# Kernel optimization log

Hardware: AMD Instinct MI355X
Metric: run time of the kernel (lower is better)

The kernel has to match this reference:

```python
import jax, jax.numpy as jnp
import numpy as np
from jax import lax

SEQ, B, I, H, O = 512, 64, 512, 1024, 512


def _linear_params(key, out_f, in_f):
    kw, kb = jax.random.split(key)
    bound = 1.0 / np.sqrt(in_f)
    W = jax.random.uniform(kw, (out_f, in_f), jnp.float32, -bound, bound)
    b = jax.random.uniform(kb, (out_f,), jnp.float32, -bound, bound)
    return W, b


def setup_inputs() -> dict:
    key = jax.random.key(0)
    ks = jax.random.split(key, 8)
    x = jax.random.normal(ks[0], (SEQ, B, I), jnp.float32)
    Wxz, bxz = _linear_params(ks[1], H, I)
    Whz, bhz = _linear_params(ks[2], H, H)
    Wxr, bxr = _linear_params(ks[3], H, I)
    Whr, bhr = _linear_params(ks[4], H, H)
    Wxh, bxh = _linear_params(ks[5], H, I)
    Whh, bhh = _linear_params(ks[6], H, H)
    Why, bhy = _linear_params(ks[7], O, H)
    return {"x": x, "Wxz": Wxz, "bxz": bxz, "Whz": Whz, "bhz": bhz,
            "Wxr": Wxr, "bxr": bxr, "Whr": Whr, "bhr": bhr,
            "Wxh": Wxh, "bxh": bxh, "Whh": Whh, "bhh": bhh,
            "Why": Why, "bhy": bhy}


def reference(x, Wxz, bxz, Whz, bhz, Wxr, bxr, Whr, bhr, Wxh, bxh, Whh, bhh, Why, bhy):
    # Precompute all input-side projections in batched GEMMs: [S,B,H]
    xz = jnp.einsum('sbi,hi->sbh', x, Wxz) + bxz
    xr = jnp.einsum('sbi,hi->sbh', x, Wxr) + bxr
    xh = jnp.einsum('sbi,hi->sbh', x, Wxh) + bxh

    def step(h, inp):
        xz_t, xr_t, xh_t = inp
        z = jax.nn.sigmoid(xz_t + h @ Whz.T + bhz)
        r = jax.nn.sigmoid(xr_t + h @ Whr.T + bhr)
        h_cand = jnp.tanh(xh_t + r * (h @ Whh.T + bhh))
        h_new = (1.0 - z) * h + z * h_cand
        return h_new, h_new

    h0 = jnp.zeros((x.shape[1], Whz.shape[0]), x.dtype)
    _, hs = lax.scan(step, h0, (xz, xr, xh))  # hs: [S,B,H]
    out = jnp.einsum('sbh,oh->sbo', hs, Why) + bhy  # [S,B,O]
    return out
```

## Files before the change

### kernel.cpp

```cpp
#include <hip/hip_runtime.h>
#include <hip/hip_bf16.h>

#define SEQL 512
#define BATCH 64
#define INF 512
#define HID 1024
#define OUTF 512
#define SB (SEQL*BATCH)
#define BH (BATCH*HID)

typedef __attribute__((ext_vector_type(8))) __bf16 bf16x8;
typedef __attribute__((ext_vector_type(4))) float f32x4;

__device__ inline bf16x8 ld_bf8(const void* p) { return *reinterpret_cast<const bf16x8*>(p); }
__device__ inline unsigned short f2bf(float f) { __bf16 b = (__bf16)f; return __builtin_bit_cast(unsigned short, b); }

__device__ inline void st_u64c(void* p, unsigned long long v) {
    __hip_atomic_store((unsigned long long*)p, v, __ATOMIC_RELAXED, __HIP_MEMORY_SCOPE_AGENT);
}

__global__ void cvt_f32_bf16(const float* __restrict__ src, unsigned short* __restrict__ dst, int n) {
    int i = (blockIdx.x * blockDim.x + threadIdx.x) * 4;
    if (i < n) {
        float4 v = *reinterpret_cast<const float4*>(src + i);
        ushort4 o = make_ushort4(f2bf(v.x), f2bf(v.y), f2bf(v.z), f2bf(v.w));
        *reinterpret_cast<ushort4*>(dst + i) = o;
    }
}

__global__ void make_bias2(const float* bxz, const float* bhz, const float* bxr,
                           const float* bhr, float* bias2) {
    int i = blockIdx.x * blockDim.x + threadIdx.x;
    if (i < HID) bias2[i] = bxz[i] + bhz[i];
    else if (i < 2*HID) bias2[i] = bxr[i-HID] + bhr[i-HID];
}

__global__ void fail_sentinel(float* o) { o[0] = 1e9f; }

__global__ __launch_bounds__(256, 2) void gemm_nt_f32(
        const unsigned short* __restrict__ A,
        const unsigned short* __restrict__ Bw, int ldb,
        const float* __restrict__ bias,
        float* __restrict__ Cf, int N, int K) {
    __shared__ __align__(16) char lds[32768];
    const int tid = threadIdx.x;
    const int ntn = N >> 7;
    const int bm = blockIdx.x / ntn, bn = blockIdx.x % ntn;
    const int rowbase = bm << 7, colbase = bn << 7;
    const int wave = tid >> 6, lane = tid & 63, lo = lane & 15, hi = lane >> 4;
    const int vm = wave >> 1, vn = wave & 1;

    auto stage = [&](int abase, int k0) {
        #pragma unroll
        for (int i = 0; i < 2; i++) {
            int linear = i * 256 + tid;
            int r = linear >> 2, s = linear & 3;
            int c = (s - (r >> 1)) & 3;
            int R = rowbase + r;
            const unsigned short* ga = A + ((size_t)(R >> 6) * 65536 + (size_t)((R >> 4) & 3) * 16384
                                     + (size_t)((((k0 + c * 8) >> 3) * 16) + (R & 15)) * 8);
            const unsigned short* gb = Bw + (size_t)(colbase + r) * ldb + k0 + c * 8;
            __builtin_amdgcn_global_load_lds(
                (const __attribute__((address_space(1))) unsigned int*)ga,
                (__attribute__((address_space(3))) unsigned int*)(lds + abase + linear * 16), 16, 0, 0);
            __builtin_amdgcn_global_load_lds(
                (const __attribute__((address_space(1))) unsigned int*)gb,
                (__attribute__((address_space(3))) unsigned int*)(lds + 16384 + abase + linear * 16), 16, 0, 0);
        }
    };

    f32x4 acc[4][4] = {};
    const int nk = K >> 5;
    stage(0, 0);
    for (int kt = 0; kt < nk; kt++) {
        __syncthreads();
        if (kt + 1 < nk) stage(((kt + 1) & 1) * 8192, (kt + 1) << 5);
        const char* cA = lds + (kt & 1) * 8192;
        const char* cB = lds + 16384 + (kt & 1) * 8192;
        bf16x8 af[4], bfr[4];
        #pragma unroll
        for (int m = 0; m < 4; m++) {
            int r = vm * 64 + m * 16 + lo;
            af[m] = ld_bf8(cA + r * 64 + 16 * ((hi + (r >> 1)) & 3));
        }
        #pragma unroll
        for (int n = 0; n < 4; n++) {
            int r = vn * 64 + n * 16 + lo;
            bfr[n] = ld_bf8(cB + r * 64 + 16 * ((hi + (r >> 1)) & 3));
        }
        #pragma unroll
        for (int m = 0; m < 4; m++)
            #pragma unroll
            for (int n = 0; n < 4; n++)
                acc[m][n] = __builtin_amdgcn_mfma_f32_16x16x32_bf16(af[m], bfr[n], acc[m][n], 0, 0, 0);
        __syncthreads();
    }

    #pragma unroll
    for (int n = 0; n < 4; n++) {
        int col = colbase + vn * 64 + n * 16 + lo;
        float bv = bias[col];
        #pragma unroll
        for (int m = 0; m < 4; m++)
            #pragma unroll
            for (int r = 0; r < 4; r++) {
                int row = rowbase + vm * 64 + m * 16 + hi * 4 + r;
                Cf[(size_t)row * N + col] = acc[m][n][r] + bv;
            }
    }
}

__global__ __launch_bounds__(192, 1) void gru_scan(
        const unsigned short* __restrict__ Whc,
        const unsigned short* __restrict__ Wxc,
        const unsigned short* __restrict__ xbf,
        unsigned short* __restrict__ hsFM,
        const float* __restrict__ bias2,
        const float* __restrict__ bxh,
        const float* __restrict__ bhh,
        unsigned int* flags) {
    __shared__ __align__(16) char lds[134656];
    const int tid = threadIdx.x;
    const int wid = blockIdx.x;
    const int rb = wid >> 6;
    const int cb = wid & 63;
    const int g = tid / 64;
    const int lane = tid & 63, lo = lane & 15, hi = lane >> 4;
    const int col = cb * 16 + lo;
    char* whl = lds + g * 32768;
    char* hstage = lds + 98304;
    f32x4* Px = (f32x4*)(lds + 131072);
    unsigned short* T = (unsigned short*)(lds + 134144);

    {
        const unsigned short* ph = Whc + ((size_t)g * HID + col) * HID + hi * 8;
        #pragma unroll
        for (int kb = 0; kb < 32; kb++)
            __builtin_amdgcn_global_load_lds(
                (const __attribute__((address_space(1))) unsigned int*)(ph + kb * 32),
                (__attribute__((address_space(3))) unsigned int*)(whl + kb * 1024 + lane * 16), 16, 0, 0);
    }
    __syncthreads();
    asm volatile("buffer_inv sc0 sc1" ::: "memory");

    const float bzv  = bias2[col];
    const float brv  = bias2[HID + col];
    const float bxhv = bxh[col];
    const float bhhv = bhh[col];
    float hst[4] = {0.f, 0.f, 0.f, 0.f};
    const unsigned short* wxp = Wxc + ((size_t)g * HID + col) * INF + hi * 8;
    const unsigned int* flA = flags + rb * 64 + (lane & 31);
    const unsigned int* flB = flags + rb * 64 + 32 + (lane & 31);

    f32x4 ax = {0,0,0,0};
    {
        const unsigned short* xp = xbf + ((size_t)(rb * 16 + lo)) * INF + hi * 8;
        #pragma unroll
        for (int kb = 0; kb < 16; kb++)
            ax = __builtin_amdgcn_mfma_f32_16x16x32_bf16(ld_bf8(xp + kb * 32), ld_bf8(wxp + kb * 32), ax, 0, 0, 0);
    }

    for (int t = 0; t < SEQL; t++) {
        if (t > 0) {
            const unsigned short* hf = hsFM + (size_t)t * 65536 + rb * 16384;
            #pragma unroll
            for (int it = 0; it < 6; it++) {
                int v = it * 192 + tid;
                if (v < 1024)
                    __builtin_amdgcn_global_load_lds(
                        (const __attribute__((address_space(1))) unsigned int*)(hf + v * 8),
                        (__attribute__((address_space(3))) unsigned int*)(hstage + v * 16), 16, 0, 0);
            }
            {
                unsigned int tgt = (unsigned int)t;
                while (!__all(__hip_atomic_load(flB, __ATOMIC_RELAXED, __HIP_MEMORY_SCOPE_AGENT) >= tgt))
                    __builtin_amdgcn_s_sleep(1);
                asm volatile("" ::: "memory");
            }
            #pragma unroll
            for (int it = 0; it < 6; it++) {
                int v = 1024 + it * 192 + tid;
                if (v < 2048)
                    __builtin_amdgcn_global_load_lds(
                        (const __attribute__((address_space(1))) unsigned int*)(hf + v * 8),
                        (__attribute__((address_space(3))) unsigned int*)(hstage + v * 16), 16, 0, 0);
            }
        }
        __syncthreads();

        f32x4 ah = {0,0,0,0};
        if (t > 0) {
            #pragma unroll
            for (int kb = 0; kb < 32; kb++) {
                bf16x8 w = ld_bf8(whl + kb * 1024 + lane * 16);
                bf16x8 a = ld_bf8(hstage + kb * 1024 + lane * 16);
                ah = __builtin_amdgcn_mfma_f32_16x16x32_bf16(a, w, ah, 0, 0, 0);
            }
        }

        if (g == 1) {
            f32x4 v;
            #pragma unroll
            for (int r = 0; r < 4; r++) v[r] = ah[r] + ax[r] + brv;
            Px[0 * 64 + lane] = v;
        } else if (g == 2) {
            f32x4 v, w;
            #pragma unroll
            for (int r = 0; r < 4; r++) { v[r] = ah[r] + bhhv; w[r] = ax[r] + bxhv; }
            Px[1 * 64 + lane] = v;
            Px[2 * 64 + lane] = w;
        }
        __syncthreads();

        if (g == 0) {
            f32x4 pr = Px[0 * 64 + lane];
            f32x4 ph_ = Px[1 * 64 + lane];
            f32x4 px_ = Px[2 * 64 + lane];
            #pragma unroll
            for (int r = 0; r < 4; r++) {
                float z  = 1.f / (1.f + __expf(-(ah[r] + ax[r] + bzv)));
                float rr = 1.f / (1.f + __expf(-pr[r]));
                float hc = tanhf(px_[r] + rr * ph_[r]);
                hst[r] = (1.f - z) * hst[r] + z * hc;
                T[(hi * 4 + r) * 16 + lo] = f2bf(hst[r]);
            }
            asm volatile("s_waitcnt lgkmcnt(0)" ::: "memory");
            unsigned short* fmdst = hsFM + (size_t)(t + 1) * 65536 + rb * 16384 + cb * 256;
            st_u64c(fmdst + lane * 4,
                    *(const unsigned long long*)(T + ((lane >> 1) & 15) * 16 + (lane >> 5) * 8 + (lane & 1) * 4));
            asm volatile("s_waitcnt vmcnt(0)" ::: "memory");
        }
        if (tid == 0)
            __hip_atomic_store(flags + rb * 64 + cb, (unsigned int)(t + 1),
                               __ATOMIC_RELAXED, __HIP_MEMORY_SCOPE_AGENT);

        f32x4 nax = {0,0,0,0};
        if (t + 1 < SEQL) {
            const unsigned short* xp = xbf + ((size_t)(t + 1) * BATCH + rb * 16 + lo) * INF + hi * 8;
            #pragma unroll
            for (int kb = 0; kb < 16; kb++)
                nax = __builtin_amdgcn_mfma_f32_16x16x32_bf16(ld_bf8(xp + kb * 32), ld_bf8(wxp + kb * 32), nax, 0, 0, 0);
            unsigned int tgt = (unsigned int)(t + 1);
            while (!__all(__hip_atomic_load(flA, __ATOMIC_RELAXED, __HIP_MEMORY_SCOPE_AGENT) >= tgt))
                __builtin_amdgcn_s_sleep(1);
            asm volatile("" ::: "memory");
        }
        ax = nax;
    }
}

extern "C" void kernel_launch(void* const* d_in, const int* in_sizes, int n_in,
                              void* d_out, int out_size, void* d_ws, size_t ws_size,
                              hipStream_t stream) {
    const float* x   = (const float*)d_in[0];
    const float* Wxz = (const float*)d_in[1];
    const float* bxz = (const float*)d_in[2];
    const float* Whz = (const float*)d_in[3];
    const float* bhz = (const float*)d_in[4];
    const float* Wxr = (const float*)d_in[5];
    const float* bxr = (const float*)d_in[6];
    const float* Whr = (const float*)d_in[7];
    const float* bhr = (const float*)d_in[8];
    const float* Wxh = (const float*)d_in[9];
    const float* bxh = (const float*)d_in[10];
    const float* Whh = (const float*)d_in[11];
    const float* bhh = (const float*)d_in[12];
    const float* Why = (const float*)d_in[13];
    const float* bhy = (const float*)d_in[14];

    char* ws = (char*)d_ws;
    size_t off = 0;
    auto alloc = [&](size_t bytes) { char* p = ws + off; off += (bytes + 255) & ~(size_t)255; return p; };
    unsigned short* Whc   = (unsigned short*)alloc((size_t)3 * HID * HID * 2);
    unsigned short* Wxc   = (unsigned short*)alloc((size_t)3 * HID * INF * 2);
    unsigned short* Whyb  = (unsigned short*)alloc((size_t)OUTF * HID * 2);
    float*          bias2 = (float*)alloc((size_t)2 * HID * 4);
    unsigned short* hsFM  = (unsigned short*)alloc((size_t)(SEQL + 1) * 65536 * 2);
    unsigned int*   flags = (unsigned int*)alloc(1024);
    unsigned short* x_bf  = (unsigned short*)d_out;

    if (off > ws_size) {
        fail_sentinel<<<dim3(1), dim3(1), 0, stream>>>((float*)d_out);
        return;
    }

    auto cvt = [&](const float* s, unsigned short* d, size_t n) {
        cvt_f32_bf16<<<dim3((unsigned)((n / 4 + 255) / 256)), dim3(256), 0, stream>>>(s, d, (int)n);
    };
    cvt(x, x_bf, (size_t)SB * INF);
    cvt(Whz, Whc, (size_t)HID * HID);
    cvt(Whr, Whc + (size_t)HID * HID, (size_t)HID * HID);
    cvt(Whh, Whc + (size_t)2 * HID * HID, (size_t)HID * HID);
    cvt(Wxz, Wxc, (size_t)HID * INF);
    cvt(Wxr, Wxc + (size_t)HID * INF, (size_t)HID * INF);
    cvt(Wxh, Wxc + (size_t)2 * HID * INF, (size_t)HID * INF);
    cvt(Why, Whyb, (size_t)OUTF * HID);
    make_bias2<<<dim3(8), dim3(256), 0, stream>>>(bxz, bhz, bxr, bhr, bias2);
    (void)hipMemsetAsync(flags, 0, 1024, stream);

    gru_scan<<<dim3(256), dim3(192), 0, stream>>>(Whc, Wxc, x_bf, hsFM, bias2, bxh, bhh, flags);

    gemm_nt_f32<<<dim3((SB / 128) * (OUTF / 128)), dim3(256), 0, stream>>>(
        hsFM + 65536, Whyb, HID, bhy, (float*)d_out, OUTF, HID);
}
```

Before: 2.857 ms.

## Prefetch next-step x tile into LDS in fragment-major layout during recurrence

Converts x to bf16 in a fragment-major layout so each 16-row block's tile is contiguous. The scan kernel then async-loads the next timestep's x tile into a new LDS stage alongside the h load, and computes the input projection from LDS before the gate math instead of after the flag store. This is meant to take the strided global x loads off the serial critical path between timesteps. The cost is about 16KB more LDS and extra MFMA work placed before the h-state publish.

```diff
diff --git a/kernel.cpp b/kernel.cpp
--- a/kernel.cpp
+++ b/kernel.cpp
@@ -11,6 +11,7 @@
 
 typedef __attribute__((ext_vector_type(8))) __bf16 bf16x8;
 typedef __attribute__((ext_vector_type(4))) float f32x4;
+typedef __attribute__((ext_vector_type(8))) unsigned short us8;
 
 __device__ inline bf16x8 ld_bf8(const void* p) { return *reinterpret_cast<const bf16x8*>(p); }
 __device__ inline unsigned short f2bf(float f) { __bf16 b = (__bf16)f; return __builtin_bit_cast(unsigned short, b); }
@@ -26,6 +27,17 @@
         ushort4 o = make_ushort4(f2bf(v.x), f2bf(v.y), f2bf(v.z), f2bf(v.w));
         *reinterpret_cast<ushort4*>(dst + i) = o;
     }
+}
+
+__global__ void cvt_x_fm(const float* __restrict__ x, unsigned short* __restrict__ xFM) {
+    int u = blockIdx.x * blockDim.x + threadIdx.x;
+    int t = u >> 12, rb = (u >> 10) & 3, v = u & 1023;
+    int row = v & 15, slot = v >> 4;
+    const float* src = x + ((size_t)(t * 64 + rb * 16 + row) * INF + slot * 8);
+    float4 a = *reinterpret_cast<const float4*>(src);
+    float4 b = *reinterpret_cast<const float4*>(src + 4);
+    us8 o = { f2bf(a.x), f2bf(a.y), f2bf(a.z), f2bf(a.w), f2bf(b.x), f2bf(b.y), f2bf(b.z), f2bf(b.w) };
+    *reinterpret_cast<us8*>(xFM + (size_t)u * 8) = o;
 }
 
 __global__ void make_bias2(const float* bxz, const float* bhz, const float* bxr,
@@ -113,13 +125,13 @@
 __global__ __launch_bounds__(192, 1) void gru_scan(
         const unsigned short* __restrict__ Whc,
         const unsigned short* __restrict__ Wxc,
-        const unsigned short* __restrict__ xbf,
+        const unsigned short* __restrict__ xFM,
         unsigned short* __restrict__ hsFM,
         const float* __restrict__ bias2,
         const float* __restrict__ bxh,
         const float* __restrict__ bhh,
         unsigned int* flags) {
-    __shared__ __align__(16) char lds[134656];
+    __shared__ __align__(16) char lds[151040];
     const int tid = threadIdx.x;
     const int wid = blockIdx.x;
     const int rb = wid >> 6;
@@ -129,8 +141,9 @@
     const int col = cb * 16 + lo;
     char* whl = lds + g * 32768;
     char* hstage = lds + 98304;
-    f32x4* Px = (f32x4*)(lds + 131072);
-    unsigned short* T = (unsigned short*)(lds + 134144);
+    char* xstage = lds + 131072;
+    f32x4* Px = (f32x4*)(lds + 147456);
+    unsigned short* T = (unsigned short*)(lds + 150528);
 
     {
         const unsigned short* ph = Whc + ((size_t)g * HID + col) * HID + hi * 8;
@@ -154,10 +167,12 @@
 
     f32x4 ax = {0,0,0,0};
     {
-        const unsigned short* xp = xbf + ((size_t)(rb * 16 + lo)) * INF + hi * 8;
-        #pragma unroll
-        for (int kb = 0; kb < 16; kb++)
-            ax = __builtin_amdgcn_mfma_f32_16x16x32_bf16(ld_bf8(xp + kb * 32), ld_bf8(wxp + kb * 32), ax, 0, 0, 0);
+        const unsigned short* xf0 = xFM + ((size_t)rb << 13);
+        #pragma unroll
+        for (int kb = 0; kb < 16; kb++) {
+            bf16x8 a = ld_bf8(xf0 + (size_t)(((kb * 4 + hi) * 16) + lo) * 8);
+            ax = __builtin_amdgcn_mfma_f32_16x16x32_bf16(a, ld_bf8(wxp + kb * 32), ax, 0, 0, 0);
+        }
     }
 
     for (int t = 0; t < SEQL; t++) {
@@ -171,12 +186,26 @@
                         (const __attribute__((address_space(1))) unsigned int*)(hf + v * 8),
                         (__attribute__((address_space(3))) unsigned int*)(hstage + v * 16), 16, 0, 0);
             }
+        }
+        if (t + 1 < SEQL) {
+            const unsigned short* xf = xFM + (((size_t)(t + 1) * 4 + rb) << 13);
+            #pragma unroll
+            for (int it = 0; it < 6; it++) {
+                int v = it * 192 + tid;
+                if (v < 1024)
+                    __builtin_amdgcn_global_load_lds(
+                        (const __attribute__((address_space(1))) unsigned int*)(xf + v * 8),
+                        (__attribute__((address_space(3))) unsigned int*)(xstage + v * 16), 16, 0, 0);
+            }
+        }
+        if (t > 0) {
             {
                 unsigned int tgt = (unsigned int)t;
                 while (!__all(__hip_atomic_load(flB, __ATOMIC_RELAXED, __HIP_MEMORY_SCOPE_AGENT) >= tgt))
                     __builtin_amdgcn_s_sleep(1);
                 asm volatile("" ::: "memory");
             }
+            const unsigned short* hf = hsFM + (size_t)t * 65536 + rb * 16384;
             #pragma unroll
             for (int it = 0; it < 6; it++) {
                 int v = 1024 + it * 192 + tid;
@@ -197,6 +226,14 @@
                 ah = __builtin_amdgcn_mfma_f32_16x16x32_bf16(a, w, ah, 0, 0, 0);
             }
         }
+        f32x4 nax = {0,0,0,0};
+        if (t + 1 < SEQL) {
+            #pragma unroll
+            for (int kb = 0; kb < 16; kb++) {
+                bf16x8 a = ld_bf8(xstage + kb * 1024 + lane * 16);
+                nax = __builtin_amdgcn_mfma_f32_16x16x32_bf16(a, ld_bf8(wxp + kb * 32), nax, 0, 0, 0);
+            }
+        }
 
         if (g == 1) {
             f32x4 v;
@@ -234,12 +271,7 @@
             __hip_atomic_store(flags + rb * 64 + cb, (unsigned int)(t + 1),
                                __ATOMIC_RELAXED, __HIP_MEMORY_SCOPE_AGENT);
 
-        f32x4 nax = {0,0,0,0};
         if (t + 1 < SEQL) {
-            const unsigned short* xp = xbf + ((size_t)(t + 1) * BATCH + rb * 16 + lo) * INF + hi * 8;
-            #pragma unroll
-            for (int kb = 0; kb < 16; kb++)
-                nax = __builtin_amdgcn_mfma_f32_16x16x32_bf16(ld_bf8(xp + kb * 32), ld_bf8(wxp + kb * 32), nax, 0, 0, 0);
             unsigned int tgt = (unsigned int)(t + 1);
             while (!__all(__hip_atomic_load(flA, __ATOMIC_RELAXED, __HIP_MEMORY_SCOPE_AGENT) >= tgt))
                 __builtin_amdgcn_s_sleep(1);
@@ -277,7 +309,7 @@
     float*          bias2 = (float*)alloc((size_t)2 * HID * 4);
     unsigned short* hsFM  = (unsigned short*)alloc((size_t)(SEQL + 1) * 65536 * 2);
     unsigned int*   flags = (unsigned int*)alloc(1024);
-    unsigned short* x_bf  = (unsigned short*)d_out;
+    unsigned short* xFM   = (unsigned short*)d_out;
 
     if (off > ws_size) {
         fail_sentinel<<<dim3(1), dim3(1), 0, stream>>>((float*)d_out);
@@ -287,7 +319,7 @@
     auto cvt = [&](const float* s, unsigned short* d, size_t n) {
         cvt_f32_bf16<<<dim3((unsigned)((n / 4 + 255) / 256)), dim3(256), 0, stream>>>(s, d, (int)n);
     };
-    cvt(x, x_bf, (size_t)SB * INF);
+    cvt_x_fm<<<dim3(8192), dim3(256), 0, stream>>>(x, xFM);
     cvt(Whz, Whc, (size_t)HID * HID);
     cvt(Whr, Whc + (size_t)HID * HID, (size_t)HID * HID);
     cvt(Whh, Whc + (size_t)2 * HID * HID, (size_t)HID * HID);
@@ -298,7 +330,7 @@
     make_bias2<<<dim3(8), dim3(256), 0, stream>>>(bxz, bhz, bxr, bhr, bias2);
     (void)hipMemsetAsync(flags, 0, 1024, stream);
 
-    gru_scan<<<dim3(256), dim3(192), 0, stream>>>(Whc, Wxc, x_bf, hsFM, bias2, bxh, bhh, flags);
+    gru_scan<<<dim3(256), dim3(192), 0, stream>>>(Whc, Wxc, xFM, hsFM, bias2, bxh, bhh, flags);
 
     gemm_nt_f32<<<dim3((SB / 128) * (OUTF / 128)), dim3(256), 0, stream>>>(
         hsFM + 65536, Whyb, HID, bhy, (float*)d_out, OUTF, HID);
```

New measurement: 3.545 ms. +24.1%, slower.
